# Kernel optimization log

Measured on AMD Instinct MI355X. Metric: run time of the kernel, lower is better.

Reference implementation:

```python
import jax, jax.numpy as jnp
import numpy as np

NEG_INF = -jnp.inf


def setup_inputs() -> dict:
    B, V = 128, 128000
    key = jax.random.key(0)
    k1, k2, k3, k4, k5 = jax.random.split(key, 5)
    logits = jax.random.normal(k1, (B, V), dtype=jnp.float32)
    # temperatures in [0.1, 1.0) to avoid divide-by-tiny blowups
    temperatures = jax.random.uniform(k2, (B,), dtype=jnp.float32) * 0.9 + 0.1
    # min_p typically small, in [0, 0.1)
    min_ps = jax.random.uniform(k3, (B,), dtype=jnp.float32) * 0.1
    # top_p in [0.1, 1.0)
    top_ps = jax.random.uniform(k4, (B,), dtype=jnp.float32) * 0.9 + 0.1
    # top_k in [1, 1000)
    top_ks = jax.random.randint(k5, (B,), 1, 1000, dtype=jnp.int32)
    return {"logits": logits, "temperatures": temperatures, "min_ps": min_ps,
            "top_ps": top_ps, "top_ks": top_ks}


def _apply_top_k_top_p(logits, top_ps, top_ks):
    B, V = logits.shape
    sort_idx = jnp.argsort(logits, axis=-1)  # ascending, matches torch sort(descending=False)
    logits_sort = jnp.take_along_axis(logits, sort_idx, axis=-1)
    # top-k: threshold is the (V-k)-th smallest value; mask anything strictly below it
    thresh_idx = (V - top_ks.astype(jnp.int32))[:, None]          # [B,1]
    thresh = jnp.take_along_axis(logits_sort, thresh_idx, axis=-1)  # [B,1]
    logits_sort = jnp.where(logits_sort < thresh, NEG_INF, logits_sort)
    # top-p: drop smallest tokens whose cumulative prob <= 1 - p; never drop the max token
    probs_sort = jax.nn.softmax(logits_sort, axis=-1)
    probs_sum = jnp.cumsum(probs_sort, axis=-1)
    top_p_mask = probs_sum <= (1.0 - top_ps)[:, None]
    top_p_mask = top_p_mask.at[:, -1].set(False)
    logits_sort = jnp.where(top_p_mask, NEG_INF, logits_sort)
    # scatter back to original vocab order
    rows = jnp.arange(B)[:, None]
    return jnp.zeros_like(logits_sort).at[rows, sort_idx].set(logits_sort)


def _apply_min_p(logits, min_ps):
    probs = jax.nn.softmax(logits, axis=-1)
    top_probs = jnp.max(probs, axis=-1, keepdims=True)
    remove = probs < min_ps[:, None] * top_probs
    return jnp.where(remove, NEG_INF, logits)


def reference(logits, temperatures, min_ps, top_ps, top_ks):
    logits = logits.astype(jnp.float32) / temperatures[:, None]
    logits = _apply_top_k_top_p(logits, top_ps, top_ks)
    logits = _apply_min_p(logits, min_ps)
    # torch.multinomial(softmax(logits), 1) == categorical sampling from logits
    sample_key = jax.random.key(42)
    next_tokens = jax.random.categorical(sample_key, logits, axis=-1)  # [B]
    return next_tokens
```

## Files before the change

kernel.cpp:

```cpp
#include <hip/hip_runtime.h>
#include <stdint.h>

#define HBINS 8192
#define HSHIFT 19
#define CAND 2048
#define NSLICES 16
#define RTHREADS 1024
#define CTHREADS 256
#define STHREADS 1024

typedef unsigned int u32;
typedef unsigned long long u64;

__device__ __forceinline__ u32 f2s(float f) {
  u32 b = __float_as_uint(f);
  return b ^ ((b & 0x80000000u) ? 0xFFFFFFFFu : 0x80000000u);
}
__device__ __forceinline__ float s2f(u32 s) {
  u32 b = (s & 0x80000000u) ? (s ^ 0x80000000u) : ~s;
  return __uint_as_float(b);
}
__device__ __forceinline__ u32 rotl32(u32 x, int r) { return (x << r) | (x >> (32 - r)); }

__device__ __forceinline__ u64 shfl_xor_u64(u64 v, int mask) {
  int lo = __shfl_xor((int)(u32)v, mask, 64);
  int hi = __shfl_xor((int)(u32)(v >> 32), mask, 64);
  return ((u64)(u32)hi << 32) | (u32)lo;
}
__device__ __forceinline__ u64 shfl_down_u64(u64 v, int delta) {
  int lo = __shfl_down((int)(u32)v, delta, 64);
  int hi = __shfl_down((int)(u32)(v >> 32), delta, 64);
  return ((u64)(u32)hi << 32) | (u32)lo;
}

__device__ __forceinline__ u32 threefry_bits(u32 ctr) {
  const u32 ks0 = 0u, ks1 = 42u, ks2 = 0x1BD11BDAu ^ 0u ^ 42u;
  u32 x0 = ks0;
  u32 x1 = ctr + ks1;
#define TFR(r) { x0 += x1; x1 = rotl32(x1, (r)); x1 ^= x0; }
  TFR(13) TFR(15) TFR(26) TFR(6)   x0 += ks1; x1 += ks2 + 1u;
  TFR(17) TFR(29) TFR(16) TFR(24)  x0 += ks2; x1 += ks0 + 2u;
  TFR(13) TFR(15) TFR(26) TFR(6)   x0 += ks0; x1 += ks1 + 3u;
  TFR(17) TFR(29) TFR(16) TFR(24)  x0 += ks1; x1 += ks2 + 4u;
  TFR(13) TFR(15) TFR(26) TFR(6)   x0 += ks2; x1 += ks0 + 5u;
#undef TFR
  return x0 ^ x1;
}

__global__ __launch_bounds__(RTHREADS)
void rowhist_kernel(const float* __restrict__ logits,
                    const int* __restrict__ topks,
                    u32* __restrict__ gthr, u32* __restrict__ gcs,
                    u32* __restrict__ gcount, int V) {
  const int row = blockIdx.x;
  const int tid = threadIdx.x;
  __shared__ u32 hp[2 * HBINS];
  __shared__ u32 part[RTHREADS];
  __shared__ int sh_pstar;

  for (int i = tid; i < 2 * HBINS; i += RTHREADS) hp[i] = 0u;
  __syncthreads();

  const float* src = logits + (size_t)row * (size_t)V;
  const u32 c = (u32)(tid & 1);
  const int n4 = V >> 2;
  const float4* p4 = (const float4*)src;
  for (int i = tid; i < n4; i += RTHREADS) {
    float4 w = p4[i];
    atomicAdd(&hp[((f2s(w.x) >> HSHIFT) << 1) | c], 1u);
    atomicAdd(&hp[((f2s(w.y) >> HSHIFT) << 1) | c], 1u);
    atomicAdd(&hp[((f2s(w.z) >> HSHIFT) << 1) | c], 1u);
    atomicAdd(&hp[((f2s(w.w) >> HSHIFT) << 1) | c], 1u);
  }
  for (int i = (n4 << 2) + tid; i < V; i += RTHREADS)
    atomicAdd(&hp[((f2s(src[i]) >> HSHIFT) << 1) | c], 1u);
  __syncthreads();

  {
    u32 s = 0;
#pragma unroll
    for (int j = 0; j < 16; ++j) s += hp[tid * 16 + j];
    part[tid] = s;
  }
  __syncthreads();
  for (int st = 1; st < RTHREADS; st <<= 1) {
    u32 v = (tid + st < RTHREADS) ? part[tid + st] : 0u;
    __syncthreads();
    part[tid] += v;
    __syncthreads();
  }

  int k = topks[row];
  if (k < 1) k = 1;
  if (k > V) k = V;
  const u32 ku = (u32)k;

  if (part[tid] >= ku && (tid == RTHREADS - 1 || part[tid + 1] < ku))
    sh_pstar = tid;
  __syncthreads();
  const int pstar = sh_pstar;
  const u32 tail = (pstar < RTHREADS - 1) ? part[pstar + 1] : 0u;
  if (tid < 8) {
    u32 sb = tail;
    for (int j = 7; j >= tid; --j) sb += hp[(pstar * 8 + j) * 2] + hp[(pstar * 8 + j) * 2 + 1];
    u32 own = hp[(pstar * 8 + tid) * 2] + hp[(pstar * 8 + tid) * 2 + 1];
    if (sb >= ku && (tid == 7 || sb - own < ku)) {
      gthr[row] = (u32)(pstar * 8 + tid) << HSHIFT;
      gcs[row] = (sb < (u32)CAND) ? sb : (u32)CAND;
      gcount[row] = 0u;
    }
  }
}

__global__ __launch_bounds__(CTHREADS)
void collect_kernel(const float* __restrict__ logits,
                    const float* __restrict__ temps,
                    const u32* __restrict__ gthr,
                    u32* __restrict__ gcount,
                    u64* __restrict__ gcand, int V, int slice_len) {
  const int row = blockIdx.x / NSLICES;
  const int sl  = blockIdx.x % NSLICES;
  const int tid = threadIdx.x;

  __shared__ u64 stage[CAND];
  __shared__ int sh_cnt, sh_base;
  if (tid == 0) sh_cnt = 0;
  __syncthreads();

  const u32 thr = gthr[row];
  const float t = temps[row];
  int rem = V - sl * slice_len;
  if (rem > slice_len) rem = slice_len;
  if (rem < 0) rem = 0;
  const float* src = logits + (size_t)row * (size_t)V + (size_t)sl * slice_len;
  const u32 ibase = (u32)(sl * slice_len);
  const int n4 = rem >> 2;
  const float4* p4 = (const float4*)src;
  for (int i = tid; i < n4; i += CTHREADS) {
    float4 w = p4[i];
    if (f2s(w.x) >= thr) { int pos = atomicAdd(&sh_cnt, 1); if (pos < CAND) stage[pos] = ((u64)f2s(w.x / t) << 32) | (ibase + 4u * i + 0u); }
    if (f2s(w.y) >= thr) { int pos = atomicAdd(&sh_cnt, 1); if (pos < CAND) stage[pos] = ((u64)f2s(w.y / t) << 32) | (ibase + 4u * i + 1u); }
    if (f2s(w.z) >= thr) { int pos = atomicAdd(&sh_cnt, 1); if (pos < CAND) stage[pos] = ((u64)f2s(w.z / t) << 32) | (ibase + 4u * i + 2u); }
    if (f2s(w.w) >= thr) { int pos = atomicAdd(&sh_cnt, 1); if (pos < CAND) stage[pos] = ((u64)f2s(w.w / t) << 32) | (ibase + 4u * i + 3u); }
  }
  for (int i = (n4 << 2) + tid; i < rem; i += CTHREADS) {
    float l = src[i];
    if (f2s(l) >= thr) { int pos = atomicAdd(&sh_cnt, 1); if (pos < CAND) stage[pos] = ((u64)f2s(l / t) << 32) | (ibase + (u32)i); }
  }
  __syncthreads();
  int n = sh_cnt;
  if (n > CAND) n = CAND;
  if (tid == 0) sh_base = (int)atomicAdd(&gcount[row], (u32)n);
  __syncthreads();
  const int base = sh_base;
  u64* gc = gcand + (size_t)row * CAND;
  for (int i = tid; i < n; i += CTHREADS) {
    int dst = base + i;
    if (dst < CAND) gc[dst] = stage[i];
  }
}

__global__ __launch_bounds__(STHREADS)
void Sampler_73529840107542_kernel(const float* __restrict__ minps,
                                   const float* __restrict__ topps,
                                   const int* __restrict__ topks,
                                   const u32* __restrict__ gcs,
                                   const u64* __restrict__ gcand,
                                   int* __restrict__ out, int V) {
  const int b = blockIdx.x;
  const int tid = threadIdx.x;
  const int w = tid >> 6;
  const int l = tid & 63;
  const float one_minus_p = 1.0f - topps[b];
  const float minp = minps[b];
  int k = topks[b];
  if (k < 1) k = 1;
  if (k > V) k = V;

  __shared__ __align__(16) unsigned char arena[34816];
  u64* cand   = (u64*)(arena);
  float* bufA = (float*)(arena + 16384);
  float* bufB = (float*)(arena + 24576);
  unsigned char* keepf = arena + 32768;
  u64* red64  = (u64*)(arena + 16384);
  float* redA = (float*)(arena + 16384);
  float* redB = (float*)(arena + 24576);

  __shared__ int sh_lb;
  __shared__ u32 sh_Ts;
  __shared__ float sh_m, sh_Z1, sh_Z2;

  const int cs = (int)gcs[b];
  const u64* gc = gcand + (size_t)b * CAND;
  const int e_lo = (w << 7) + l;
  const int e_hi = e_lo + 64;
  const u64 SENT = 0xFFFFFFFFFFFFFFFFull;
  u64 k0 = (e_lo < cs) ? gc[e_lo] : SENT;
  u64 k1 = (e_hi < cs) ? gc[e_hi] : SENT;

  int P = 64;
  while (P < cs) P <<= 1;
  for (int size = 2; size <= P; size <<= 1) {
    for (int s = size >> 1; s > 0; s >>= 1) {
      if (s >= 128) {
        cand[e_lo] = k0; cand[e_hi] = k1;
        __syncthreads();
        u64 p0 = cand[e_lo ^ s], p1 = cand[e_hi ^ s];
        {
          bool keepmin = (((e_lo & s) == 0) == ((e_lo & size) == 0));
          if (keepmin ? (p0 < k0) : (p0 > k0)) k0 = p0;
        }
        {
          bool keepmin = (((e_hi & s) == 0) == ((e_hi & size) == 0));
          if (keepmin ? (p1 < k1) : (p1 > k1)) k1 = p1;
        }
        __syncthreads();
      } else if (s == 64) {
        bool asc = ((e_lo & size) == 0);
        if ((k0 > k1) == asc) { u64 t = k0; k0 = k1; k1 = t; }
      } else {
        u64 p0 = shfl_xor_u64(k0, s);
        u64 p1 = shfl_xor_u64(k1, s);
        {
          bool keepmin = (((l & s) == 0) == ((e_lo & size) == 0));
          if (keepmin ? (p0 < k0) : (p0 > k0)) k0 = p0;
        }
        {
          bool keepmin = (((l & s) == 0) == ((e_hi & size) == 0));
          if (keepmin ? (p1 < k1) : (p1 > k1)) k1 = p1;
        }
      }
    }
  }
  cand[e_lo] = k0; cand[e_hi] = k1;
  __syncthreads();

  if (tid == 0) {
    int ti = cs - k; if (ti < 0) ti = 0;
    sh_Ts = (u32)(cand[ti] >> 32);
    sh_m  = s2f((u32)(cand[cs - 1] >> 32));
  }
  __syncthreads();
  const u32 Ts = sh_Ts;
  const float m = sh_m;

  for (int c = tid; c < cs; c += STHREADS) {
    u32 s = (u32)(cand[c] >> 32);
    if (s >= Ts && (c == 0 || (u32)(cand[c - 1] >> 32) < Ts)) sh_lb = c;
  }
  __syncthreads();
  const int lb = sh_lb;

  {
    float e0 = 0.0f, e1 = 0.0f;
    const int c0 = tid, c1 = tid + STHREADS;
    if (c0 < cs) {
      u32 s = (u32)(cand[c0] >> 32);
      if (s >= Ts) e0 = expf(s2f(s) - m);
    }
    if (c1 < cs) {
      u32 s = (u32)(cand[c1] >> 32);
      if (s >= Ts) e1 = expf(s2f(s) - m);
    }
    bufA[c0] = e0;
    bufA[c1] = e1;
    redB[tid] = e0 + e1;
  }
  __syncthreads();
  for (int s = STHREADS >> 1; s >= 64; s >>= 1) {
    if (tid < s) redB[tid] += redB[tid + s];
    __syncthreads();
  }
  if (w == 0) {
    float v = redB[l];
    v += __shfl_down(v, 32, 64);
    v += __shfl_down(v, 16, 64);
    v += __shfl_down(v, 8, 64);
    v += __shfl_down(v, 4, 64);
    v += __shfl_down(v, 2, 64);
    v += __shfl_down(v, 1, 64);
    if (l == 0) sh_Z1 = v;
  }
  __syncthreads();
  const float Z1 = sh_Z1;

  if (w == 0) {
    float carry = 0.0f;
    for (int base = lb; base < cs; base += 64) {
      int c = base + l;
      float v = (c < cs) ? bufA[c] / Z1 : 0.0f;
      u32 vb = __float_as_uint(v);
      float acc = carry;
#pragma unroll
      for (int j = 0; j < 64; ++j) {
        float t = __uint_as_float(__builtin_amdgcn_readlane(vb, j));
        acc += (l >= j) ? t : 0.0f;
      }
      if (c < cs) bufB[c] = acc;
      carry = __uint_as_float(__builtin_amdgcn_readlane(__float_as_uint(acc), 63));
    }
  }
  __syncthreads();

  {
    float local = 0.0f;
    for (int c = tid; c < CAND; c += STHREADS) {
      unsigned char kf = 0;
      if (c < cs) {
        u32 s = (u32)(cand[c] >> 32);
        if (s >= Ts && (c == cs - 1 || bufB[c] > one_minus_p)) kf = 1;
        if (kf) local += expf(s2f(s) - m);
      }
      keepf[c] = kf;
    }
    redA[tid] = local;
  }
  __syncthreads();
  for (int s = STHREADS >> 1; s >= 64; s >>= 1) {
    if (tid < s) redA[tid] += redA[tid + s];
    __syncthreads();
  }
  if (w == 0) {
    float v = redA[l];
    v += __shfl_down(v, 32, 64);
    v += __shfl_down(v, 16, 64);
    v += __shfl_down(v, 8, 64);
    v += __shfl_down(v, 4, 64);
    v += __shfl_down(v, 2, 64);
    v += __shfl_down(v, 1, 64);
    if (l == 0) sh_Z2 = v;
  }
  __syncthreads();

  {
    const float Z2 = sh_Z2;
    const float rhs = minp * (1.0f / Z2);
    for (int c = tid; c < CAND; c += STHREADS) {
      if (keepf[c]) {
        u32 s = (u32)(cand[c] >> 32);
        float p2 = expf(s2f(s) - m) / Z2;
        if (p2 < rhs) keepf[c] = 0;
      }
    }
  }
  __syncthreads();

  {
    const float TINY = 1.17549435082228750797e-38f;
    u64 best = 0ull;
    for (int c = lb + tid; c < cs; c += STHREADS) {
      if (!keepf[c]) continue;
      u32 s = (u32)(cand[c] >> 32);
      u32 idx = (u32)(cand[c] & 0xFFFFFFFFull);
      float x = s2f(s);
      u32 bits = threefry_bits((u32)b * (u32)V + idx);
      float f = __uint_as_float((bits >> 9) | 0x3f800000u) - 1.0f;
      float u = fmaxf(TINY, f * 1.0f + TINY);
      float g = -logf(-logf(u));
      float sc = g + x;
      u64 key = ((u64)f2s(sc) << 32) | (u64)(0xFFFFFFFFu - idx);
      if (key > best) best = key;
    }
    red64[tid] = best;
    __syncthreads();
    for (int s = STHREADS >> 1; s >= 64; s >>= 1) {
      if (tid < s) { u64 o = red64[tid + s]; if (o > red64[tid]) red64[tid] = o; }
      __syncthreads();
    }
    if (w == 0) {
      u64 v = red64[l];
#pragma unroll
      for (int d = 32; d >= 1; d >>= 1) {
        u64 o = shfl_down_u64(v, d);
        if (o > v) v = o;
      }
      if (l == 0) out[b] = (int)(0xFFFFFFFFu - (u32)(v & 0xFFFFFFFFull));
    }
  }
}

extern "C" void kernel_launch(void* const* d_in, const int* in_sizes, int n_in,
                              void* d_out, int out_size, void* d_ws, size_t ws_size,
                              hipStream_t stream) {
  const float* logits = (const float*)d_in[0];
  const float* temps  = (const float*)d_in[1];
  const float* minps  = (const float*)d_in[2];
  const float* topps  = (const float*)d_in[3];
  const int*   topks  = (const int*)d_in[4];
  const int B = in_sizes[1];
  const int V = in_sizes[0] / B;
  (void)n_in; (void)out_size; (void)ws_size;

  u32* gcount = (u32*)d_ws;
  u32* gcs    = gcount + B;
  u32* gthr   = gcs + B;
  u64* gcand  = (u64*)(gthr + B);

  const int slice_len = (((V + NSLICES - 1) / NSLICES) + 3) & ~3;

  rowhist_kernel<<<dim3(B), dim3(RTHREADS), 0, stream>>>(
      logits, topks, gthr, gcs, gcount, V);
  collect_kernel<<<dim3(B * NSLICES), dim3(CTHREADS), 0, stream>>>(
      logits, temps, gthr, gcount, gcand, V, slice_len);
  Sampler_73529840107542_kernel<<<dim3(B), dim3(STHREADS), 0, stream>>>(
      minps, topps, topks, gcs, gcand, (int*)d_out, V);
}
```

Baseline: 165.5 us.

## Fuse histogram, candidate collection and sampling into one per-row kernel

Merges the three kernels (row histogram, sliced candidate collection, sampler) into a single 1024-thread block per row. The threshold and candidate list now stay in shared memory instead of going through global workspace, which removes two launches and the global candidate round trip. In exchange, the collection pass that used 16 slices per row now runs as one block per row with 128 blocks total, so it has less parallelism. Shared memory per block also grows to about 68KB, which can limit occupancy.

```diff
diff --git a/kernel.cpp b/kernel.cpp
--- a/kernel.cpp
+++ b/kernel.cpp
@@ -4,9 +4,6 @@
 #define HBINS 8192
 #define HSHIFT 19
 #define CAND 2048
-#define NSLICES 16
-#define RTHREADS 1024
-#define CTHREADS 256
 #define STHREADS 1024
 
 typedef unsigned int u32;
@@ -47,138 +44,22 @@
   return x0 ^ x1;
 }
 
-__global__ __launch_bounds__(RTHREADS)
-void rowhist_kernel(const float* __restrict__ logits,
-                    const int* __restrict__ topks,
-                    u32* __restrict__ gthr, u32* __restrict__ gcs,
-                    u32* __restrict__ gcount, int V) {
-  const int row = blockIdx.x;
-  const int tid = threadIdx.x;
-  __shared__ u32 hp[2 * HBINS];
-  __shared__ u32 part[RTHREADS];
-  __shared__ int sh_pstar;
-
-  for (int i = tid; i < 2 * HBINS; i += RTHREADS) hp[i] = 0u;
-  __syncthreads();
-
-  const float* src = logits + (size_t)row * (size_t)V;
-  const u32 c = (u32)(tid & 1);
-  const int n4 = V >> 2;
-  const float4* p4 = (const float4*)src;
-  for (int i = tid; i < n4; i += RTHREADS) {
-    float4 w = p4[i];
-    atomicAdd(&hp[((f2s(w.x) >> HSHIFT) << 1) | c], 1u);
-    atomicAdd(&hp[((f2s(w.y) >> HSHIFT) << 1) | c], 1u);
-    atomicAdd(&hp[((f2s(w.z) >> HSHIFT) << 1) | c], 1u);
-    atomicAdd(&hp[((f2s(w.w) >> HSHIFT) << 1) | c], 1u);
-  }
-  for (int i = (n4 << 2) + tid; i < V; i += RTHREADS)
-    atomicAdd(&hp[((f2s(src[i]) >> HSHIFT) << 1) | c], 1u);
-  __syncthreads();
-
-  {
-    u32 s = 0;
-#pragma unroll
-    for (int j = 0; j < 16; ++j) s += hp[tid * 16 + j];
-    part[tid] = s;
-  }
-  __syncthreads();
-  for (int st = 1; st < RTHREADS; st <<= 1) {
-    u32 v = (tid + st < RTHREADS) ? part[tid + st] : 0u;
-    __syncthreads();
-    part[tid] += v;
-    __syncthreads();
-  }
-
-  int k = topks[row];
-  if (k < 1) k = 1;
-  if (k > V) k = V;
-  const u32 ku = (u32)k;
-
-  if (part[tid] >= ku && (tid == RTHREADS - 1 || part[tid + 1] < ku))
-    sh_pstar = tid;
-  __syncthreads();
-  const int pstar = sh_pstar;
-  const u32 tail = (pstar < RTHREADS - 1) ? part[pstar + 1] : 0u;
-  if (tid < 8) {
-    u32 sb = tail;
-    for (int j = 7; j >= tid; --j) sb += hp[(pstar * 8 + j) * 2] + hp[(pstar * 8 + j) * 2 + 1];
-    u32 own = hp[(pstar * 8 + tid) * 2] + hp[(pstar * 8 + tid) * 2 + 1];
-    if (sb >= ku && (tid == 7 || sb - own < ku)) {
-      gthr[row] = (u32)(pstar * 8 + tid) << HSHIFT;
-      gcs[row] = (sb < (u32)CAND) ? sb : (u32)CAND;
-      gcount[row] = 0u;
-    }
-  }
-}
-
-__global__ __launch_bounds__(CTHREADS)
-void collect_kernel(const float* __restrict__ logits,
-                    const float* __restrict__ temps,
-                    const u32* __restrict__ gthr,
-                    u32* __restrict__ gcount,
-                    u64* __restrict__ gcand, int V, int slice_len) {
-  const int row = blockIdx.x / NSLICES;
-  const int sl  = blockIdx.x % NSLICES;
-  const int tid = threadIdx.x;
-
-  __shared__ u64 stage[CAND];
-  __shared__ int sh_cnt, sh_base;
-  if (tid == 0) sh_cnt = 0;
-  __syncthreads();
-
-  const u32 thr = gthr[row];
-  const float t = temps[row];
-  int rem = V - sl * slice_len;
-  if (rem > slice_len) rem = slice_len;
-  if (rem < 0) rem = 0;
-  const float* src = logits + (size_t)row * (size_t)V + (size_t)sl * slice_len;
-  const u32 ibase = (u32)(sl * slice_len);
-  const int n4 = rem >> 2;
-  const float4* p4 = (const float4*)src;
-  for (int i = tid; i < n4; i += CTHREADS) {
-    float4 w = p4[i];
-    if (f2s(w.x) >= thr) { int pos = atomicAdd(&sh_cnt, 1); if (pos < CAND) stage[pos] = ((u64)f2s(w.x / t) << 32) | (ibase + 4u * i + 0u); }
-    if (f2s(w.y) >= thr) { int pos = atomicAdd(&sh_cnt, 1); if (pos < CAND) stage[pos] = ((u64)f2s(w.y / t) << 32) | (ibase + 4u * i + 1u); }
-    if (f2s(w.z) >= thr) { int pos = atomicAdd(&sh_cnt, 1); if (pos < CAND) stage[pos] = ((u64)f2s(w.z / t) << 32) | (ibase + 4u * i + 2u); }
-    if (f2s(w.w) >= thr) { int pos = atomicAdd(&sh_cnt, 1); if (pos < CAND) stage[pos] = ((u64)f2s(w.w / t) << 32) | (ibase + 4u * i + 3u); }
-  }
-  for (int i = (n4 << 2) + tid; i < rem; i += CTHREADS) {
-    float l = src[i];
-    if (f2s(l) >= thr) { int pos = atomicAdd(&sh_cnt, 1); if (pos < CAND) stage[pos] = ((u64)f2s(l / t) << 32) | (ibase + (u32)i); }
-  }
-  __syncthreads();
-  int n = sh_cnt;
-  if (n > CAND) n = CAND;
-  if (tid == 0) sh_base = (int)atomicAdd(&gcount[row], (u32)n);
-  __syncthreads();
-  const int base = sh_base;
-  u64* gc = gcand + (size_t)row * CAND;
-  for (int i = tid; i < n; i += CTHREADS) {
-    int dst = base + i;
-    if (dst < CAND) gc[dst] = stage[i];
-  }
-}
-
 __global__ __launch_bounds__(STHREADS)
-void Sampler_73529840107542_kernel(const float* __restrict__ minps,
+void Sampler_73529840107542_kernel(const float* __restrict__ logits,
+                                   const float* __restrict__ temps,
+                                   const float* __restrict__ minps,
                                    const float* __restrict__ topps,
                                    const int* __restrict__ topks,
-                                   const u32* __restrict__ gcs,
-                                   const u64* __restrict__ gcand,
                                    int* __restrict__ out, int V) {
-  const int b = blockIdx.x;
+  const int row = blockIdx.x;
   const int tid = threadIdx.x;
   const int w = tid >> 6;
   const int l = tid & 63;
-  const float one_minus_p = 1.0f - topps[b];
-  const float minp = minps[b];
-  int k = topks[b];
-  if (k < 1) k = 1;
-  if (k > V) k = V;
-
-  __shared__ __align__(16) unsigned char arena[34816];
-  u64* cand   = (u64*)(arena);
+
+  __shared__ __align__(16) unsigned char arena[69632];
+  u32* hp     = (u32*)arena;
+  u32* part   = (u32*)(arena + 65536);
+  u64* cand   = (u64*)arena;
   float* bufA = (float*)(arena + 16384);
   float* bufB = (float*)(arena + 24576);
   unsigned char* keepf = arena + 32768;
@@ -186,17 +67,87 @@
   float* redA = (float*)(arena + 16384);
   float* redB = (float*)(arena + 24576);
 
-  __shared__ int sh_lb;
-  __shared__ u32 sh_Ts;
+  __shared__ int sh_pstar, sh_cnt, sh_lb, sh_cs;
+  __shared__ u32 sh_thr, sh_Ts;
   __shared__ float sh_m, sh_Z1, sh_Z2;
 
-  const int cs = (int)gcs[b];
-  const u64* gc = gcand + (size_t)b * CAND;
+  for (int i = tid; i < 2 * HBINS; i += STHREADS) hp[i] = 0u;
+  __syncthreads();
+  const float* src = logits + (size_t)row * (size_t)V;
+  const u32 pc = (u32)(tid & 1);
+  const int n4 = V >> 2;
+  const float4* p4 = (const float4*)src;
+  for (int i = tid; i < n4; i += STHREADS) {
+    float4 v = p4[i];
+    atomicAdd(&hp[((f2s(v.x) >> HSHIFT) << 1) | pc], 1u);
+    atomicAdd(&hp[((f2s(v.y) >> HSHIFT) << 1) | pc], 1u);
+    atomicAdd(&hp[((f2s(v.z) >> HSHIFT) << 1) | pc], 1u);
+    atomicAdd(&hp[((f2s(v.w) >> HSHIFT) << 1) | pc], 1u);
+  }
+  for (int i = (n4 << 2) + tid; i < V; i += STHREADS)
+    atomicAdd(&hp[((f2s(src[i]) >> HSHIFT) << 1) | pc], 1u);
+  __syncthreads();
+
+  {
+    u32 s = 0;
+#pragma unroll
+    for (int j = 0; j < 16; ++j) s += hp[tid * 16 + j];
+    part[tid] = s;
+  }
+  __syncthreads();
+  for (int st = 1; st < STHREADS; st <<= 1) {
+    u32 v = (tid + st < STHREADS) ? part[tid + st] : 0u;
+    __syncthreads();
+    part[tid] += v;
+    __syncthreads();
+  }
+  int k = topks[row];
+  if (k < 1) k = 1;
+  if (k > V) k = V;
+  const u32 ku = (u32)k;
+  if (part[tid] >= ku && (tid == STHREADS - 1 || part[tid + 1] < ku))
+    sh_pstar = tid;
+  __syncthreads();
+  {
+    const int pstar = sh_pstar;
+    const u32 tail = (pstar < STHREADS - 1) ? part[pstar + 1] : 0u;
+    if (tid < 8) {
+      u32 sb = tail;
+      for (int j = 7; j >= tid; --j) sb += hp[(pstar * 8 + j) * 2] + hp[(pstar * 8 + j) * 2 + 1];
+      u32 own = hp[(pstar * 8 + tid) * 2] + hp[(pstar * 8 + tid) * 2 + 1];
+      if (sb >= ku && (tid == 7 || sb - own < ku)) {
+        sh_thr = (u32)(pstar * 8 + tid) << HSHIFT;
+        sh_cs = (int)((sb < (u32)CAND) ? sb : (u32)CAND);
+      }
+    }
+    if (tid == 0) sh_cnt = 0;
+  }
+  __syncthreads();
+
+  const u32 thr = sh_thr;
+  const float t = temps[row];
+  for (int i = tid; i < n4; i += STHREADS) {
+    float4 v = p4[i];
+    if (f2s(v.x) >= thr) { int pos = atomicAdd(&sh_cnt, 1); if (pos < CAND) cand[pos] = ((u64)f2s(v.x / t) << 32) | (u32)(4 * i + 0); }
+    if (f2s(v.y) >= thr) { int pos = atomicAdd(&sh_cnt, 1); if (pos < CAND) cand[pos] = ((u64)f2s(v.y / t) << 32) | (u32)(4 * i + 1); }
+    if (f2s(v.z) >= thr) { int pos = atomicAdd(&sh_cnt, 1); if (pos < CAND) cand[pos] = ((u64)f2s(v.z / t) << 32) | (u32)(4 * i + 2); }
+    if (f2s(v.w) >= thr) { int pos = atomicAdd(&sh_cnt, 1); if (pos < CAND) cand[pos] = ((u64)f2s(v.w / t) << 32) | (u32)(4 * i + 3); }
+  }
+  for (int i = (n4 << 2) + tid; i < V; i += STHREADS) {
+    float x = src[i];
+    if (f2s(x) >= thr) { int pos = atomicAdd(&sh_cnt, 1); if (pos < CAND) cand[pos] = ((u64)f2s(x / t) << 32) | (u32)i; }
+  }
+  __syncthreads();
+  const int cs = sh_cs;
+
+  const float one_minus_p = 1.0f - topps[row];
+  const float minp = minps[row];
   const int e_lo = (w << 7) + l;
   const int e_hi = e_lo + 64;
   const u64 SENT = 0xFFFFFFFFFFFFFFFFull;
-  u64 k0 = (e_lo < cs) ? gc[e_lo] : SENT;
-  u64 k1 = (e_hi < cs) ? gc[e_hi] : SENT;
+  u64 k0 = (e_lo < cs) ? cand[e_lo] : SENT;
+  u64 k1 = (e_hi < cs) ? cand[e_hi] : SENT;
+  __syncthreads();
 
   int P = 64;
   while (P < cs) P <<= 1;
@@ -217,7 +168,7 @@
         __syncthreads();
       } else if (s == 64) {
         bool asc = ((e_lo & size) == 0);
-        if ((k0 > k1) == asc) { u64 t = k0; k0 = k1; k1 = t; }
+        if ((k0 > k1) == asc) { u64 tt = k0; k0 = k1; k1 = tt; }
       } else {
         u64 p0 = shfl_xor_u64(k0, s);
         u64 p1 = shfl_xor_u64(k1, s);
@@ -293,8 +244,8 @@
       float acc = carry;
 #pragma unroll
       for (int j = 0; j < 64; ++j) {
-        float t = __uint_as_float(__builtin_amdgcn_readlane(vb, j));
-        acc += (l >= j) ? t : 0.0f;
+        float tt = __uint_as_float(__builtin_amdgcn_readlane(vb, j));
+        acc += (l >= j) ? tt : 0.0f;
       }
       if (c < cs) bufB[c] = acc;
       carry = __uint_as_float(__builtin_amdgcn_readlane(__float_as_uint(acc), 63));
@@ -353,7 +304,7 @@
       u32 s = (u32)(cand[c] >> 32);
       u32 idx = (u32)(cand[c] & 0xFFFFFFFFull);
       float x = s2f(s);
-      u32 bits = threefry_bits((u32)b * (u32)V + idx);
+      u32 bits = threefry_bits((u32)row * (u32)V + idx);
       float f = __uint_as_float((bits >> 9) | 0x3f800000u) - 1.0f;
       float u = fmaxf(TINY, f * 1.0f + TINY);
       float g = -logf(-logf(u));
@@ -374,7 +325,7 @@
         u64 o = shfl_down_u64(v, d);
         if (o > v) v = o;
       }
-      if (l == 0) out[b] = (int)(0xFFFFFFFFu - (u32)(v & 0xFFFFFFFFull));
+      if (l == 0) out[row] = (int)(0xFFFFFFFFu - (u32)(v & 0xFFFFFFFFull));
     }
   }
 }
@@ -389,19 +340,8 @@
   const int*   topks  = (const int*)d_in[4];
   const int B = in_sizes[1];
   const int V = in_sizes[0] / B;
-  (void)n_in; (void)out_size; (void)ws_size;
-
-  u32* gcount = (u32*)d_ws;
-  u32* gcs    = gcount + B;
-  u32* gthr   = gcs + B;
-  u64* gcand  = (u64*)(gthr + B);
-
-  const int slice_len = (((V + NSLICES - 1) / NSLICES) + 3) & ~3;
-
-  rowhist_kernel<<<dim3(B), dim3(RTHREADS), 0, stream>>>(
-      logits, topks, gthr, gcs, gcount, V);
-  collect_kernel<<<dim3(B * NSLICES), dim3(CTHREADS), 0, stream>>>(
-      logits, temps, gthr, gcount, gcand, V, slice_len);
+  (void)n_in; (void)out_size; (void)d_ws; (void)ws_size;
+
   Sampler_73529840107542_kernel<<<dim3(B), dim3(STHREADS), 0, stream>>>(
-      minps, topps, topks, gcs, gcand, (int*)d_out, V);
-}
+      logits, temps, minps, topps, topks, (int*)d_out, V);
+}
```

Result: no change. 164.0 us (-0.9%).
